# Kernel optimization log

Measured on AMD Instinct MI355X. Metric: run time of the kernel, lower is better.

The kernel has to match this reference:

```python
import jax, jax.numpy as jnp
import numpy as np

B, C, H, W = 4, 256, 48, 48
HEADS, DH = 8, 32
INNER = HEADS * DH
HID = 128  # max(16, INNER//2)
SCALE = DH ** -0.5
EPS = 1e-6


def setup_inputs() -> dict:
    key = jax.random.key(0)
    ks = jax.random.split(key, 32)
    s = 0.02
    inp = {
        'x': jax.random.normal(ks[0], (B, C, H, W), jnp.float32),
        'rgb_input': jax.random.uniform(ks[1], (B, 3, H, W), jnp.float32),
        'wq': jax.random.normal(ks[2], (INNER, C), jnp.float32) * s,
        'bq': jnp.zeros((INNER,), jnp.float32),
        'wk': jax.random.normal(ks[3], (INNER, C), jnp.float32) * s,
        'bk': jnp.zeros((INNER,), jnp.float32),
        'wv': jax.random.normal(ks[4], (INNER, C), jnp.float32) * s,
        'bv': jnp.zeros((INNER,), jnp.float32),
        'wproj': jax.random.normal(ks[5], (C, INNER), jnp.float32) * s,
        'bproj': jnp.zeros((C,), jnp.float32),
        'c1_w': jax.random.normal(ks[6], (HID, 1, 3, 3), jnp.float32) * s,
        'c1_b': jnp.zeros((HID,), jnp.float32),
        'c2_w': jax.random.normal(ks[7], (HID, HID, 3, 3), jnp.float32) * s,
        'c2_b': jnp.zeros((HID,), jnp.float32),
        'gq_w': jax.random.normal(ks[8], (INNER, HID), jnp.float32) * s,
        'gq_b': jnp.ones((INNER,), jnp.float32),
        'bqf_w': jax.random.normal(ks[9], (INNER, HID), jnp.float32) * s,
        'bqf_b': jnp.zeros((INNER,), jnp.float32),
        'gk_w': jax.random.normal(ks[10], (INNER, HID), jnp.float32) * s,
        'gk_b': jnp.ones((INNER,), jnp.float32),
        'bkf_w': jax.random.normal(ks[11], (INNER, HID), jnp.float32) * s,
        'bkf_b': jnp.zeros((INNER,), jnp.float32),
        'gv_w': jax.random.normal(ks[12], (INNER, HID), jnp.float32) * s,
        'gv_b': jnp.ones((INNER,), jnp.float32),
        'bvf_w': jax.random.normal(ks[13], (INNER, HID), jnp.float32) * s,
        'bvf_b': jnp.zeros((INNER,), jnp.float32),
        'alpha': jnp.float32(0.1),
    }
    return inp


def _conv3(x, w, b):
    y = jax.lax.conv_general_dilated(x, w, (1, 1), 'SAME',
                                     dimension_numbers=('NCHW', 'OIHW', 'NCHW'))
    return y + b[None, :, None, None]


def _rgb_to_luma(rgb):
    y = 0.299 * rgb[:, 0:1] + 0.587 * rgb[:, 1:2] + 0.114 * rgb[:, 2:3]
    y_min = jnp.min(y, axis=(2, 3), keepdims=True)
    y_max = jnp.max(y, axis=(2, 3), keepdims=True)
    return (y - y_min) / (y_max - y_min + EPS)


def reference(x, rgb_input, wq, bq, wk, bk, wv, bv, wproj, bproj,
              c1_w, c1_b, c2_w, c2_b,
              gq_w, gq_b, bqf_w, bqf_b, gk_w, gk_b, bkf_w, bkf_b,
              gv_w, gv_b, bvf_w, bvf_b, alpha):
    Bx, Cx, Hx, Wx = x.shape
    N = Hx * Wx
    luma = _rgb_to_luma(rgb_input)  # [B,1,H,W]

    # LumaCond trunk + FiLM params (1x1 convs then global spatial mean)
    h = jax.nn.relu(_conv3(luma, c1_w, c1_b))
    h = jax.nn.relu(_conv3(h, c2_w, c2_b))
    hm = h.mean(axis=(2, 3))  # [B,HID] (mean commutes with 1x1 conv)

    def film_params(gw, gb, bw, bb):
        g = hm @ gw.T + gb  # [B, INNER]
        bta = hm @ bw.T + bb
        return (g.reshape(Bx, HEADS, DH, 1), bta.reshape(Bx, HEADS, DH, 1))

    gq, fbq = film_params(gq_w, gq_b, bqf_w, bqf_b)
    gk, fbk = film_params(gk_w, gk_b, bkf_w, bkf_b)
    gv, fbv = film_params(gv_w, gv_b, bvf_w, bvf_b)

    def proj_film(w, b, g, bta):
        t = jnp.einsum('bchw,oc->bohw', x, w) + b[None, :, None, None]
        t = t.reshape(Bx, HEADS, DH, N)
        return g * t + bta  # [B,heads,dh,N]

    q = proj_film(wq, bq, gq, fbq)
    k = proj_film(wk, bk, gk, fbk)
    v = proj_film(wv, bv, gv, fbv)

    logits = jnp.einsum('bhdn,bhdm->bhnm', q, k) * SCALE  # [B,heads,N,N]

    # luma bias: avg-pooled inverse luma, mean-centered per image
    invL = 1.0 - luma
    invL = jax.lax.reduce_window(invL, 0.0, jax.lax.add,
                                 (1, 1, 3, 3), (1, 1, 1, 1), 'SAME') / 9.0
    invL = invL.reshape(Bx, N)
    invL = invL - invL.mean(axis=-1, keepdims=True)
    logits = logits + alpha * invL[:, None, None, :]

    attn = jax.nn.softmax(logits, axis=-1)
    out = jnp.einsum('bhnm,bhdm->bhdn', attn, v)  # [B,heads,dh,N]
    out = out.reshape(Bx, INNER, Hx, Wx)
    return jnp.einsum('bchw,oc->bohw', out, wproj) + bproj[None, :, None, None]
```

## Files before the change

kernel.cpp:

```cpp
#include <hip/hip_runtime.h>


#define NSP 2304
#define WID 48

typedef __attribute__((ext_vector_type(4))) float  fvec4;
typedef __attribute__((ext_vector_type(2))) unsigned int uvec2;
typedef __attribute__((ext_vector_type(4))) unsigned int uvec4;
typedef __attribute__((ext_vector_type(8))) short  short8;
typedef __attribute__((ext_vector_type(4))) float  f32x4;

__device__ inline unsigned short f2bf(float f){
  unsigned int u = __builtin_bit_cast(unsigned int, f);
  u += 0x7fffu + ((u >> 16) & 1u);
  return (unsigned short)(u >> 16);
}
__device__ inline unsigned pack2bf(float a, float b){
#if __has_builtin(__builtin_amdgcn_cvt_pk_bf16_f32)
  typedef __attribute__((ext_vector_type(2))) __bf16 bf16x2;
  bf16x2 r = __builtin_amdgcn_cvt_pk_bf16_f32(a, b);
  return __builtin_bit_cast(unsigned, r);
#else
  return (unsigned)f2bf(a) | ((unsigned)f2bf(b) << 16);
#endif
}

__global__ void k0b_wcast(const float* __restrict__ c2w, const float* __restrict__ wq,
                          const float* __restrict__ wk, const float* __restrict__ wv_,
                          const float* __restrict__ wproj,
                          unsigned short* __restrict__ wtb,
                          unsigned short* __restrict__ wqkvb,
                          unsigned short* __restrict__ wprojb){
  int idx = blockIdx.x*256 + threadIdx.x;
  if (idx < 147456){
    int ic = idx & 127, rem = idx >> 7;
    int oc = rem & 127, tap = rem >> 7;
    wtb[idx] = f2bf(c2w[(oc*128 + ic)*9 + tap]);
  } else if (idx < 344064){
    int j = idx - 147456;
    int mat = j >> 16, oc_ = j & 65535;
    const float* src = (mat == 0) ? wq : (mat == 1) ? wk : wv_;
    wqkvb[j] = f2bf(src[oc_]);
  } else {
    int j = idx - 344064;
    wprojb[j] = f2bf(wproj[j]);
  }
}

__global__ __launch_bounds__(256) void k0xt(const float* __restrict__ x,
                                            unsigned short* __restrict__ xt){
  int nt = blockIdx.x, cc = blockIdx.y, b = blockIdx.z, t = threadIdx.x;
  __shared__ unsigned short tb[64*72];
  int cl0 = t >> 4;
  int nl0 = (t & 15) * 4;
  #pragma unroll
  for (int ps = 0; ps < 4; ++ps){
    int cl = cl0 + ps*16;
    fvec4 v = *(const fvec4*)(x + ((size_t)(b*256 + cc*64 + cl))*NSP + nt*64 + nl0);
    #pragma unroll
    for (int i = 0; i < 4; ++i) tb[(nl0+i)*72 + cl] = f2bf(v[i]);
  }
  __syncthreads();
  int nl = t >> 2, cg = (t & 3) * 16;
  uvec4 u0 = *(const uvec4*)&tb[nl*72 + cg];
  uvec4 u1 = *(const uvec4*)&tb[nl*72 + cg + 8];
  unsigned short* dst = xt + ((size_t)(b*NSP + nt*64 + nl))*256 + cc*64 + cg;
  *(uvec4*)dst = u0;
  *(uvec4*)(dst + 8) = u1;
}

__global__ void k1_luma(const float* __restrict__ rgb, const float* __restrict__ alphaP,
                        float* __restrict__ luma_n, float* __restrict__ bias_a,
                        float* __restrict__ hm_sum){
  int b = blockIdx.x, t = threadIdx.x;
  __shared__ float ly[NSP];
  __shared__ float ll[NSP];
  __shared__ float red[256];
  __shared__ float red2[256];
  const float* rp = rgb + b*3*NSP;
  float lmin = 1e30f, lmax = -1e30f;
  for (int i = t; i < NSP; i += 256){
    float y = 0.299f*rp[i] + 0.587f*rp[NSP+i] + 0.114f*rp[2*NSP+i];
    ly[i] = y; lmin = fminf(lmin, y); lmax = fmaxf(lmax, y);
  }
  red[t] = lmin; red2[t] = lmax;
  __syncthreads();
  for (int s = 128; s > 0; s >>= 1){
    if (t < s){ red[t] = fminf(red[t], red[t+s]); red2[t] = fmaxf(red2[t], red2[t+s]); }
    __syncthreads();
  }
  float mn = red[0], mx = red2[0];
  float inv = 1.0f / (mx - mn + 1e-6f);
  for (int i = t; i < NSP; i += 256){
    float v = (ly[i] - mn) * inv;
    ll[i] = v;
    luma_n[b*NSP + i] = v;
  }
  if (t < 128) hm_sum[b*128 + t] = 0.f;
  __syncthreads();
  float pr[9]; float psum = 0.f;
  #pragma unroll
  for (int ii = 0; ii < 9; ++ii){
    int n = t + 256*ii;
    int row = n / WID, col = n - row*WID;
    float s = 0.f;
    #pragma unroll
    for (int dy = -1; dy <= 1; ++dy)
      #pragma unroll
      for (int dx = -1; dx <= 1; ++dx){
        int r2 = row+dy, c2 = col+dx;
        if (r2 >= 0 && r2 < WID && c2 >= 0 && c2 < WID) s += 1.0f - ll[r2*WID + c2];
      }
    pr[ii] = s * (1.f/9.f);
    psum += pr[ii];
  }
  __syncthreads();
  red[t] = psum;
  __syncthreads();
  for (int s = 128; s > 0; s >>= 1){
    if (t < s) red[t] += red[t+s];
    __syncthreads();
  }
  float mean = red[0] * (1.f/(float)NSP);
  float alpha = alphaP[0] * 1.4426950408889634f;
  #pragma unroll
  for (int ii = 0; ii < 9; ++ii){
    int n = t + 256*ii;
    bias_a[b*NSP + n] = alpha * (pr[ii] - mean);
  }
}

__global__ void k2_conv1(const float* __restrict__ luma_n, const float* __restrict__ c1w,
                         const float* __restrict__ c1b, unsigned short* __restrict__ h1p){
  int nt = blockIdx.x, ocg = blockIdx.y, b = blockIdx.z, t = threadIdx.x;
  __shared__ float wsm[32*9];
  __shared__ float bsm[32];
  for (int i = t; i < 288; i += 256) wsm[i] = c1w[ocg*288 + i];
  if (t < 32) bsm[t] = c1b[ocg*32 + t];
  __syncthreads();
  int n = nt*256 + t;
  int row = n / WID, col = n - row*WID;
  const float* lp = luma_n + b*NSP;
  float lv[9];
  int k = 0;
  #pragma unroll
  for (int dy = -1; dy <= 1; ++dy)
    #pragma unroll
    for (int dx = -1; dx <= 1; ++dx, ++k){
      int r2 = row+dy, c2 = col+dx;
      lv[k] = (r2 >= 0 && r2 < WID && c2 >= 0 && c2 < WID) ? lp[r2*WID + c2] : 0.f;
    }
  unsigned int packed[16];
  #pragma unroll
  for (int oc2 = 0; oc2 < 16; ++oc2){
    float a0 = bsm[oc2*2], a1 = bsm[oc2*2+1];
    #pragma unroll
    for (int q = 0; q < 9; ++q){
      a0 += wsm[(oc2*2)*9 + q] * lv[q];
      a1 += wsm[(oc2*2+1)*9 + q] * lv[q];
    }
    packed[oc2] = pack2bf(fmaxf(a0, 0.f), fmaxf(a1, 0.f));
  }
  unsigned short* dst = h1p + ((size_t)(b*2500 + (row+1)*50 + (col+1)))*128 + ocg*32;
  #pragma unroll
  for (int q4 = 0; q4 < 4; ++q4)
    *(uvec4*)(dst + q4*8) = *(uvec4*)&packed[q4*4];
}

__global__ __launch_bounds__(256) void k3_conv2(const unsigned short* __restrict__ h1p,
    const unsigned short* __restrict__ wtb, const float* __restrict__ c2b,
    float* __restrict__ hm_sum){
  int row = blockIdx.x, mh = blockIdx.y, b = blockIdx.z;
  int t = threadIdx.x, wv = t >> 6, lane = t & 63;
  int lq = lane >> 4, lc = lane & 15;
  int ocb = mh*64 + wv*16;
  const f32x4 z4 = {0.f, 0.f, 0.f, 0.f};
  f32x4 C[3] = {z4, z4, z4};
  const unsigned short* hbase = h1p + (size_t)b*2500*128;
  #pragma unroll
  for (int tap = 0; tap < 9; ++tap){
    int dy = tap/3 - 1, dx = tap%3 - 1;
    const unsigned short* wrow = wtb + (tap*128 + ocb + lc)*128 + lq*8;
    const unsigned short* hrow = hbase + ((row+dy+1)*50 + (dx+1) + lc)*128 + lq*8;
    #pragma unroll
    for (int kc = 0; kc < 4; ++kc){
      short8 aW = *(const short8*)(wrow + kc*32);
      #pragma unroll
      for (int ntp = 0; ntp < 3; ++ntp){
        short8 bH = *(const short8*)(hrow + ntp*16*128 + kc*32);
        C[ntp] = __builtin_amdgcn_mfma_f32_16x16x32_bf16(aW, bH, C[ntp], 0, 0, 0);
      }
    }
  }
  float s[4];
  #pragma unroll
  for (int r = 0; r < 4; ++r){
    float bias = c2b[ocb + lq*4 + r];
    float v = 0.f;
    #pragma unroll
    for (int ntp = 0; ntp < 3; ++ntp) v += fmaxf(C[ntp][r] + bias, 0.f);
    v += __shfl_xor(v, 1, 64);
    v += __shfl_xor(v, 2, 64);
    v += __shfl_xor(v, 4, 64);
    v += __shfl_xor(v, 8, 64);
    s[r] = v;
  }
  if (lc == 0){
    #pragma unroll
    for (int r = 0; r < 4; ++r)
      atomicAdd(&hm_sum[b*128 + ocb + lq*4 + r], s[r]);
  }
}

__global__ void k4_film(const float* __restrict__ hm_sum,
  const float* w0, const float* b0, const float* w1, const float* b1,
  const float* w2, const float* b2, const float* w3, const float* b3,
  const float* w4, const float* b4, const float* w5, const float* b5,
  float* __restrict__ film){
  __shared__ float hs[128];
  int bb = blockIdx.x & 3, m6 = blockIdx.x >> 2, t = threadIdx.x;
  if (t < 128) hs[t] = hm_sum[bb*128 + t] * (1.f/(float)NSP);
  __syncthreads();
  const float* wm[6] = {w0,w1,w2,w3,w4,w5};
  const float* bm[6] = {b0,b1,b2,b3,b4,b5};
  const float* w = wm[m6];
  int o = t;
  float a = bm[m6][o];
  for (int h2 = 0; h2 < 128; ++h2) a += hs[h2] * w[o*128 + h2];
  film[blockIdx.x*256 + t] = a;
}

__global__ __launch_bounds__(256) void k5_qkv(const unsigned short* __restrict__ xt,
    const unsigned short* __restrict__ wqkvb,
    const float* __restrict__ bq, const float* __restrict__ bk, const float* __restrict__ bv,
    const float* __restrict__ film,
    unsigned short* __restrict__ q_t, unsigned short* __restrict__ k_t,
    unsigned short* __restrict__ v_b){
  int nt = blockIdx.x, ot = blockIdx.y, b = blockIdx.z;
  int t = threadIdx.x, wv = t >> 6, lane = t & 63;
  int lq = lane >> 4, lc = lane & 15;
  int p = ot >> 1;
  int omb = (ot & 1)*128 + wv*32;
  const unsigned short* wb = wqkvb + p*65536;
  const f32x4 z4 = {0.f, 0.f, 0.f, 0.f};
  f32x4 acc[2][4];
  #pragma unroll
  for (int oh = 0; oh < 2; ++oh)
    #pragma unroll
    for (int nq = 0; nq < 4; ++nq) acc[oh][nq] = z4;
  for (int kc = 0; kc < 8; ++kc){
    short8 aW[2];
    #pragma unroll
    for (int oh = 0; oh < 2; ++oh)
      aW[oh] = *(const short8*)(wb + (omb + oh*16 + lc)*256 + kc*32 + lq*8);
    short8 bX[4];
    #pragma unroll
    for (int nq = 0; nq < 4; ++nq)
      bX[nq] = *(const short8*)(xt + ((size_t)(b*NSP + nt*64 + nq*16 + lc))*256 + kc*32 + lq*8);
    #pragma unroll
    for (int oh = 0; oh < 2; ++oh)
      #pragma unroll
      for (int nq = 0; nq < 4; ++nq)
        acc[oh][nq] = __builtin_amdgcn_mfma_f32_16x16x32_bf16(aW[oh], bX[nq], acc[oh][nq], 0, 0, 0);
  }
  const float* bvec = (p == 0) ? bq : (p == 1) ? bk : bv;
  int hq = omb >> 5;
  unsigned short* qk = (p == 0) ? q_t : k_t;
  #pragma unroll
  for (int oh = 0; oh < 2; ++oh){
    fvec4 g4 = *(const fvec4*)(film + (2*p*4 + b)*256 + omb + oh*16 + lq*4);
    fvec4 t4 = *(const fvec4*)(film + ((2*p+1)*4 + b)*256 + omb + oh*16 + lq*4);
    fvec4 z4b = *(const fvec4*)(bvec + omb + oh*16 + lq*4);
    #pragma unroll
    for (int nq = 0; nq < 4; ++nq){
      int n = nt*64 + nq*16 + lc;
      float v0 = g4[0]*(acc[oh][nq][0] + z4b[0]) + t4[0];
      float v1 = g4[1]*(acc[oh][nq][1] + z4b[1]) + t4[1];
      float v2 = g4[2]*(acc[oh][nq][2] + z4b[2]) + t4[2];
      float v3 = g4[3]*(acc[oh][nq][3] + z4b[3]) + t4[3];
      if (p == 0){
        const float sc = 0.17677669529663687f * 1.4426950408889634f;
        v0 *= sc; v1 *= sc; v2 *= sc; v3 *= sc;
      }
      if (p < 2){
        uvec2 u;
        u.x = pack2bf(v0, v1);
        u.y = pack2bf(v2, v3);
        *(uvec2*)(qk + ((size_t)((b*8 + hq)*NSP + n))*32 + oh*16 + lq*4) = u;
      } else {
        int om = omb + oh*16 + lq*4;
        v_b[((size_t)(b*256 + om + 0))*NSP + n] = f2bf(v0);
        v_b[((size_t)(b*256 + om + 1))*NSP + n] = f2bf(v1);
        v_b[((size_t)(b*256 + om + 2))*NSP + n] = f2bf(v2);
        v_b[((size_t)(b*256 + om + 3))*NSP + n] = f2bf(v3);
      }
    }
  }
}

__global__ __launch_bounds__(256, 4) void k6_attn(const unsigned short* __restrict__ q_t,
    const unsigned short* __restrict__ k_t, const unsigned short* __restrict__ v_b,
    const float* __restrict__ bias_a,
    unsigned short* __restrict__ o0, unsigned short* __restrict__ o1,
    float* __restrict__ l0, float* __restrict__ l1){
  int bx = blockIdx.x, h = blockIdx.y, b = blockIdx.z;
  int qblk = bx >> 1, s = bx & 1;
  unsigned short* op = s ? o1 : o0;
  float* lp = s ? l1 : l0;
  int t = threadIdx.x, wv = t >> 6, lane = t & 63;
  int lq = lane >> 4, lc = lane & 15;
  int bh = b*8 + h;
  int nb0 = qblk*128 + wv*32;
  const f32x4 z4 = {0.f, 0.f, 0.f, 0.f};
  int ms = s*1152;

  __shared__ unsigned short Kb[2][64*32];
  __shared__ unsigned short Vb[2][32*64];
  __shared__ float ps[4][1024];

  const unsigned short* kg = k_t + ((size_t)bh*NSP + ms + (t>>2))*32 + (t&3)*8;
  const unsigned short* vg = v_b + ((size_t)(b*256 + h*32 + (t>>3)))*NSP + ms + (t&7)*8;
  int krow = t >> 2;
  unsigned short* kw = &Kb[0][krow*32 + (((t&3) ^ ((krow>>1)&3))*8)];
  int vrow = t >> 3;
  unsigned short* vw = &Vb[0][vrow*64 + (((t&7) ^ (vrow&7))*8)];

  int kcol = (lq ^ ((lc>>1)&3))*8;
  int sxm = ((lc&7)<<2) | (((lc>>3)&1)<<1);
  int wbase = lc*32;

  const float* brow = bias_a + b*NSP + ms;
  fvec4 c0r[4];
  #pragma unroll
  for (int g = 0; g < 4; ++g) c0r[g] = *(const fvec4*)(brow + g*16 + lq*4);

  short8 aQ[2];
  #pragma unroll
  for (int qf = 0; qf < 2; ++qf)
    aQ[qf] = *(const short8*)(q_t + ((size_t)(bh*NSP + nb0 + qf*16 + lc))*32 + lq*8);

  uvec4 gKr = *(const uvec4*)kg;
  uvec4 gVr = *(const uvec4*)vg;

  const uvec4 onesu = {0x3F803F80u, 0x3F803F80u, 0x3F803F80u, 0x3F803F80u};
  const short8 aOnes = __builtin_bit_cast(short8, onesu);

  f32x4 O[2][2]; f32x4 Ol[2];
  #pragma unroll
  for (int qf = 0; qf < 2; ++qf){
    Ol[qf] = z4; O[qf][0] = z4; O[qf][1] = z4;
  }
  float* myps = ps[wv];

  for (int it = 0; it < 18; ++it){
    int buf = it & 1;
    *(uvec4*)(kw + buf*2048) = gKr;
    *(uvec4*)(vw + buf*2048) = gVr;
    __syncthreads();
    if (it < 17){
      gKr = *(const uvec4*)(kg + (it+1)*2048);
      gVr = *(const uvec4*)(vg + (it+1)*64);
    }
    const unsigned short* kb = Kb[buf];
    const unsigned short* vb = Vb[buf];
    short8 aK[4], aV[2][2];
    #pragma unroll
    for (int g = 0; g < 4; ++g)
      aK[g] = *(const short8*)(kb + (g*16 + lc)*32 + kcol);
    #pragma unroll
    for (int dhg = 0; dhg < 2; ++dhg)
      #pragma unroll
      for (int mh = 0; mh < 2; ++mh)
        aV[dhg][mh] = *(const short8*)(vb + (dhg*16 + lc)*64 + (((mh*4 + lq) ^ (lc&7))*8));
    #pragma unroll
    for (int qf = 0; qf < 2; ++qf){
      #pragma unroll
      for (int g = 0; g < 4; ++g){
        f32x4 S = __builtin_amdgcn_mfma_f32_16x16x32_bf16(aK[g], aQ[qf], c0r[g], 0, 0, 0);
        uvec2 w2;
        w2.x = pack2bf(__builtin_amdgcn_exp2f(S[0]), __builtin_amdgcn_exp2f(S[1]));
        w2.y = pack2bf(__builtin_amdgcn_exp2f(S[2]), __builtin_amdgcn_exp2f(S[3]));
        *(uvec2*)&myps[qf*512 + wbase + ((g*8 + lq*2) ^ sxm)] = w2;
      }
    }
    if (it < 17){
      #pragma unroll
      for (int g = 0; g < 4; ++g)
        c0r[g] = *(const fvec4*)(brow + (it+1)*64 + g*16 + lq*4);
    }
    __builtin_amdgcn_s_setprio(1);
    #pragma unroll
    for (int qf = 0; qf < 2; ++qf){
      #pragma unroll
      for (int mh = 0; mh < 2; ++mh){
        int d0 = (mh*16 + lq*4) ^ sxm;
        uvec2 lo = *(const uvec2*)&myps[qf*512 + wbase + d0];
        uvec2 hi = *(const uvec2*)&myps[qf*512 + wbase + (d0 ^ 2)];
        uvec4 up; up.x = lo.x; up.y = lo.y; up.z = hi.x; up.w = hi.y;
        short8 bP = __builtin_bit_cast(short8, up);
        Ol[qf] = __builtin_amdgcn_mfma_f32_16x16x32_bf16(aOnes, bP, Ol[qf], 0, 0, 0);
        #pragma unroll
        for (int dhg = 0; dhg < 2; ++dhg)
          O[qf][dhg] = __builtin_amdgcn_mfma_f32_16x16x32_bf16(aV[dhg][mh], bP, O[qf][dhg], 0, 0, 0);
      }
    }
    __builtin_amdgcn_s_setprio(0);
  }
  #pragma unroll
  for (int qf = 0; qf < 2; ++qf){
    int nidx = nb0 + qf*16 + lc;
    if (lq == 0) lp[b*NSP + nidx] = Ol[qf][0];
    #pragma unroll
    for (int dh = 0; dh < 2; ++dh){
      uvec2 u;
      u.x = pack2bf(O[qf][dh][0], O[qf][dh][1]);
      u.y = pack2bf(O[qf][dh][2], O[qf][dh][3]);
      *(uvec2*)(op + ((size_t)(b*NSP + nidx))*256 + h*32 + dh*16 + lq*4) = u;
    }
  }
}

__global__ __launch_bounds__(256) void k7_proj(const unsigned short* __restrict__ a0,
    const unsigned short* __restrict__ a1, const float* __restrict__ l0p,
    const float* __restrict__ l1p, const unsigned short* __restrict__ wprojb,
    const float* __restrict__ bproj, float* __restrict__ out){
  int nt = blockIdx.x, ct = blockIdx.y, b = blockIdx.z;
  int t = threadIdx.x, wv = t >> 6, lane = t & 63;
  int lq = lane >> 4, lc = lane & 15;
  __shared__ float rls[32];
  if (t < 32) rls[t] = 1.0f / (l0p[b*NSP + nt*32 + t] + l1p[b*NSP + nt*32 + t]);
  __syncthreads();
  int cb = ct*128 + wv*32;
  const f32x4 z4 = {0.f, 0.f, 0.f, 0.f};
  f32x4 acc[2][2];
  #pragma unroll
  for (int ch = 0; ch < 2; ++ch)
    #pragma unroll
    for (int nq = 0; nq < 2; ++nq) acc[ch][nq] = z4;
  for (int kc = 0; kc < 8; ++kc){
    short8 aW[2];
    #pragma unroll
    for (int ch = 0; ch < 2; ++ch)
      aW[ch] = *(const short8*)(wprojb + (cb + ch*16 + lc)*256 + kc*32 + lq*8);
    #pragma unroll
    for (int src = 0; src < 2; ++src){
      const unsigned short* ap = src ? a1 : a0;
      short8 bA[2];
      #pragma unroll
      for (int nq = 0; nq < 2; ++nq)
        bA[nq] = *(const short8*)(ap + ((size_t)(b*NSP + nt*32 + nq*16 + lc))*256 + kc*32 + lq*8);
      #pragma unroll
      for (int ch = 0; ch < 2; ++ch)
        #pragma unroll
        for (int nq = 0; nq < 2; ++nq)
          acc[ch][nq] = __builtin_amdgcn_mfma_f32_16x16x32_bf16(aW[ch], bA[nq], acc[ch][nq], 0, 0, 0);
    }
  }
  #pragma unroll
  for (int ch = 0; ch < 2; ++ch){
    #pragma unroll
    for (int nq = 0; nq < 2; ++nq){
      int n = nt*32 + nq*16 + lc;
      float rl = rls[nq*16 + lc];
      #pragma unroll
      for (int r = 0; r < 4; ++r){
        int c = cb + ch*16 + lq*4 + r;
        out[((size_t)(b*256 + c))*NSP + n] = acc[ch][nq][r]*rl + bproj[c];
      }
    }
  }
}

extern "C" void kernel_launch(void* const* d_in, const int* in_sizes, int n_in,
                              void* d_out, int out_size, void* d_ws, size_t ws_size,
                              hipStream_t stream) {
  const float* x     = (const float*)d_in[0];
  const float* rgb   = (const float*)d_in[1];
  const float* wq    = (const float*)d_in[2];
  const float* bq    = (const float*)d_in[3];
  const float* wk    = (const float*)d_in[4];
  const float* bk    = (const float*)d_in[5];
  const float* wv    = (const float*)d_in[6];
  const float* bv    = (const float*)d_in[7];
  const float* wproj = (const float*)d_in[8];
  const float* bproj = (const float*)d_in[9];
  const float* c1w   = (const float*)d_in[10];
  const float* c1b   = (const float*)d_in[11];
  const float* c2w   = (const float*)d_in[12];
  const float* c2b   = (const float*)d_in[13];
  const float* gq_w  = (const float*)d_in[14];
  const float* gq_b  = (const float*)d_in[15];
  const float* bqf_w = (const float*)d_in[16];
  const float* bqf_b = (const float*)d_in[17];
  const float* gk_w  = (const float*)d_in[18];
  const float* gk_b  = (const float*)d_in[19];
  const float* bkf_w = (const float*)d_in[20];
  const float* bkf_b = (const float*)d_in[21];
  const float* gv_w  = (const float*)d_in[22];
  const float* gv_b  = (const float*)d_in[23];
  const float* bvf_w = (const float*)d_in[24];
  const float* bvf_b = (const float*)d_in[25];
  const float* alphaP= (const float*)d_in[26];

  char* w = (char*)d_ws;
  float* luma_n = (float*)w;            w += 4*NSP*4;
  float* bias_a = (float*)w;            w += 4*NSP*4;
  float* hm_sum = (float*)w;            w += 512*4;
  float* film   = (float*)w;            w += 6*4*256*4;
  unsigned short* h1p = (unsigned short*)w; w += 4*2500*128*2;
  unsigned short* wtb = (unsigned short*)w; w += 9*128*128*2;
  unsigned short* wqkvb = (unsigned short*)w; w += 3*256*256*2;
  unsigned short* wprojb = (unsigned short*)w; w += 256*256*2;
  unsigned short* xt  = (unsigned short*)w; w += (size_t)4*NSP*256*2;
  unsigned short* q_t = (unsigned short*)w; w += (size_t)4*8*NSP*32*2;
  unsigned short* k_t = (unsigned short*)w; w += (size_t)4*8*NSP*32*2;
  unsigned short* v_b = (unsigned short*)w; w += (size_t)4*256*NSP*2;
  unsigned short* o_part0 = (unsigned short*)w; w += (size_t)4*NSP*256*2;
  unsigned short* o_part1 = (unsigned short*)w; w += (size_t)4*NSP*256*2;
  float* l_part0 = (float*)w;           w += 4*NSP*4;
  float* l_part1 = (float*)w;           w += 4*NSP*4;

  (void)hipMemsetAsync(h1p, 0, (size_t)4*2500*128*2, stream);
  k0b_wcast<<<1600, 256, 0, stream>>>(c2w, wq, wk, wv, wproj, wtb, wqkvb, wprojb);
  k0xt    <<<dim3(36,4,4), 256, 0, stream>>>(x, xt);
  k1_luma <<<4, 256, 0, stream>>>(rgb, alphaP, luma_n, bias_a, hm_sum);
  k2_conv1<<<dim3(9,4,4), 256, 0, stream>>>(luma_n, c1w, c1b, h1p);
  k3_conv2<<<dim3(48,2,4), 256, 0, stream>>>(h1p, wtb, c2b, hm_sum);
  k4_film <<<24, 256, 0, stream>>>(hm_sum, gq_w, gq_b, bqf_w, bqf_b,
                                   gk_w, gk_b, bkf_w, bkf_b,
                                   gv_w, gv_b, bvf_w, bvf_b, film);
  k5_qkv  <<<dim3(36,6,4), 256, 0, stream>>>(xt, wqkvb, bq, bk, bv, film,
                                             q_t, k_t, v_b);
  k6_attn <<<dim3(36,8,4), 256, 0, stream>>>(q_t, k_t, v_b, bias_a,
                                             o_part0, o_part1, l_part0, l_part1);
  k7_proj <<<dim3(72,2,4), 256, 0, stream>>>(o_part0, o_part1, l_part0, l_part1,
                                             wprojb, bproj, (float*)d_out);
}
```

Measured before the change: 267.5 us.

## Register-prefetch operands in GEMMs, drop LDS staging in attention, fold halo memset into luma

```diff
diff --git a/kernel.cpp b/kernel.cpp
--- a/kernel.cpp
+++ b/kernel.cpp
@@ -69,64 +69,80 @@
   *(uvec4*)(dst + 8) = u1;
 }
 
-__global__ void k1_luma(const float* __restrict__ rgb, const float* __restrict__ alphaP,
+__global__ __launch_bounds__(1024) void k1_luma(const float* __restrict__ rgb,
+                        const float* __restrict__ alphaP,
                         float* __restrict__ luma_n, float* __restrict__ bias_a,
-                        float* __restrict__ hm_sum){
+                        float* __restrict__ hm_sum, unsigned short* __restrict__ h1p){
   int b = blockIdx.x, t = threadIdx.x;
   __shared__ float ly[NSP];
   __shared__ float ll[NSP];
-  __shared__ float red[256];
-  __shared__ float red2[256];
+  __shared__ float red[1024];
+  __shared__ float red2[1024];
+  {
+    const uvec4 z = {0u,0u,0u,0u};
+    for (int j = t; j < 196*16; j += 1024){
+      int cell = j >> 4, q = j & 15;
+      int r, c;
+      if (cell < 50)      { r = 0;           c = cell; }
+      else if (cell < 100){ r = 49;          c = cell - 50; }
+      else if (cell < 148){ r = cell - 99;   c = 0; }
+      else                { r = cell - 147;  c = 49; }
+      *(uvec4*)(h1p + ((size_t)(b*2500 + r*50 + c))*128 + q*8) = z;
+    }
+  }
   const float* rp = rgb + b*3*NSP;
   float lmin = 1e30f, lmax = -1e30f;
-  for (int i = t; i < NSP; i += 256){
+  for (int i = t; i < NSP; i += 1024){
     float y = 0.299f*rp[i] + 0.587f*rp[NSP+i] + 0.114f*rp[2*NSP+i];
     ly[i] = y; lmin = fminf(lmin, y); lmax = fmaxf(lmax, y);
   }
   red[t] = lmin; red2[t] = lmax;
   __syncthreads();
-  for (int s = 128; s > 0; s >>= 1){
+  for (int s = 512; s > 0; s >>= 1){
     if (t < s){ red[t] = fminf(red[t], red[t+s]); red2[t] = fmaxf(red2[t], red2[t+s]); }
     __syncthreads();
   }
   float mn = red[0], mx = red2[0];
   float inv = 1.0f / (mx - mn + 1e-6f);
-  for (int i = t; i < NSP; i += 256){
+  for (int i = t; i < NSP; i += 1024){
     float v = (ly[i] - mn) * inv;
     ll[i] = v;
     luma_n[b*NSP + i] = v;
   }
   if (t < 128) hm_sum[b*128 + t] = 0.f;
   __syncthreads();
-  float pr[9]; float psum = 0.f;
-  #pragma unroll
-  for (int ii = 0; ii < 9; ++ii){
-    int n = t + 256*ii;
-    int row = n / WID, col = n - row*WID;
-    float s = 0.f;
-    #pragma unroll
-    for (int dy = -1; dy <= 1; ++dy)
-      #pragma unroll
-      for (int dx = -1; dx <= 1; ++dx){
-        int r2 = row+dy, c2 = col+dx;
-        if (r2 >= 0 && r2 < WID && c2 >= 0 && c2 < WID) s += 1.0f - ll[r2*WID + c2];
-      }
-    pr[ii] = s * (1.f/9.f);
-    psum += pr[ii];
+  float pr[3]; float psum = 0.f;
+  #pragma unroll
+  for (int ii = 0; ii < 3; ++ii){
+    int n = t + 1024*ii;
+    pr[ii] = 0.f;
+    if (n < NSP){
+      int row = n / WID, col = n - row*WID;
+      float s = 0.f;
+      #pragma unroll
+      for (int dy = -1; dy <= 1; ++dy)
+        #pragma unroll
+        for (int dx = -1; dx <= 1; ++dx){
+          int r2 = row+dy, c2 = col+dx;
+          if (r2 >= 0 && r2 < WID && c2 >= 0 && c2 < WID) s += 1.0f - ll[r2*WID + c2];
+        }
+      pr[ii] = s * (1.f/9.f);
+      psum += pr[ii];
+    }
   }
   __syncthreads();
   red[t] = psum;
   __syncthreads();
-  for (int s = 128; s > 0; s >>= 1){
+  for (int s = 512; s > 0; s >>= 1){
     if (t < s) red[t] += red[t+s];
     __syncthreads();
   }
   float mean = red[0] * (1.f/(float)NSP);
   float alpha = alphaP[0] * 1.4426950408889634f;
   #pragma unroll
-  for (int ii = 0; ii < 9; ++ii){
-    int n = t + 256*ii;
-    bias_a[b*NSP + n] = alpha * (pr[ii] - mean);
+  for (int ii = 0; ii < 3; ++ii){
+    int n = t + 1024*ii;
+    if (n < NSP) bias_a[b*NSP + n] = alpha * (pr[ii] - mean);
   }
 }
 
@@ -241,28 +257,41 @@
   int lq = lane >> 4, lc = lane & 15;
   int p = ot >> 1;
   int omb = (ot & 1)*128 + wv*32;
-  const unsigned short* wb = wqkvb + p*65536;
   const f32x4 z4 = {0.f, 0.f, 0.f, 0.f};
   f32x4 acc[2][4];
   #pragma unroll
   for (int oh = 0; oh < 2; ++oh)
     #pragma unroll
     for (int nq = 0; nq < 4; ++nq) acc[oh][nq] = z4;
-  for (int kc = 0; kc < 8; ++kc){
-    short8 aW[2];
+
+  const unsigned short* wbp = wqkvb + p*65536 + (omb + lc)*256 + lq*8;
+  const unsigned short* xbp = xt + ((size_t)(b*NSP + nt*64 + lc))*256 + lq*8;
+
+  short8 aW0[2], aW1[2], bX0[4], bX1[4];
+  auto loadW = [&](short8 (&W)[2], int kc){
+    #pragma unroll
+    for (int oh = 0; oh < 2; ++oh) W[oh] = *(const short8*)(wbp + oh*16*256 + kc*32);
+  };
+  auto loadX = [&](short8 (&X)[4], int kc){
+    #pragma unroll
+    for (int nq = 0; nq < 4; ++nq) X[nq] = *(const short8*)(xbp + (size_t)nq*16*256 + kc*32);
+  };
+  auto mm = [&](short8 (&W)[2], short8 (&X)[4]){
     #pragma unroll
     for (int oh = 0; oh < 2; ++oh)
-      aW[oh] = *(const short8*)(wb + (omb + oh*16 + lc)*256 + kc*32 + lq*8);
-    short8 bX[4];
-    #pragma unroll
-    for (int nq = 0; nq < 4; ++nq)
-      bX[nq] = *(const short8*)(xt + ((size_t)(b*NSP + nt*64 + nq*16 + lc))*256 + kc*32 + lq*8);
-    #pragma unroll
-    for (int oh = 0; oh < 2; ++oh)
       #pragma unroll
       for (int nq = 0; nq < 4; ++nq)
-        acc[oh][nq] = __builtin_amdgcn_mfma_f32_16x16x32_bf16(aW[oh], bX[nq], acc[oh][nq], 0, 0, 0);
-  }
+        acc[oh][nq] = __builtin_amdgcn_mfma_f32_16x16x32_bf16(W[oh], X[nq], acc[oh][nq], 0, 0, 0);
+  };
+  loadW(aW0, 0); loadX(bX0, 0);
+  for (int kc2 = 0; kc2 < 4; ++kc2){
+    loadW(aW1, kc2*2+1); loadX(bX1, kc2*2+1);
+    mm(aW0, bX0);
+    int kn = (kc2*2+2) & 7;
+    loadW(aW0, kn); loadX(bX0, kn);
+    mm(aW1, bX1);
+  }
+
   const float* bvec = (p == 0) ? bq : (p == 1) ? bk : bv;
   int hq = omb >> 5;
   unsigned short* qk = (p == 0) ? q_t : k_t;
@@ -314,33 +343,23 @@
   const f32x4 z4 = {0.f, 0.f, 0.f, 0.f};
   int ms = s*1152;
 
-  __shared__ unsigned short Kb[2][64*32];
-  __shared__ unsigned short Vb[2][32*64];
   __shared__ float ps[4][1024];
-
-  const unsigned short* kg = k_t + ((size_t)bh*NSP + ms + (t>>2))*32 + (t&3)*8;
-  const unsigned short* vg = v_b + ((size_t)(b*256 + h*32 + (t>>3)))*NSP + ms + (t&7)*8;
-  int krow = t >> 2;
-  unsigned short* kw = &Kb[0][krow*32 + (((t&3) ^ ((krow>>1)&3))*8)];
-  int vrow = t >> 3;
-  unsigned short* vw = &Vb[0][vrow*64 + (((t&7) ^ (vrow&7))*8)];
-
-  int kcol = (lq ^ ((lc>>1)&3))*8;
+  float* myps = ps[wv];
   int sxm = ((lc&7)<<2) | (((lc>>3)&1)<<1);
   int wbase = lc*32;
 
+  const unsigned short* kfr = k_t + ((size_t)(bh*NSP + ms + lc))*32 + lq*8;
+  const unsigned short* vfr = v_b + ((size_t)(b*256 + h*32 + lc))*NSP + ms + lq*8;
   const float* brow = bias_a + b*NSP + ms;
-  fvec4 c0r[4];
-  #pragma unroll
-  for (int g = 0; g < 4; ++g) c0r[g] = *(const fvec4*)(brow + g*16 + lq*4);
 
   short8 aQ[2];
   #pragma unroll
   for (int qf = 0; qf < 2; ++qf)
     aQ[qf] = *(const short8*)(q_t + ((size_t)(bh*NSP + nb0 + qf*16 + lc))*32 + lq*8);
 
-  uvec4 gKr = *(const uvec4*)kg;
-  uvec4 gVr = *(const uvec4*)vg;
+  fvec4 c0r[4];
+  #pragma unroll
+  for (int g = 0; g < 4; ++g) c0r[g] = *(const fvec4*)(brow + g*16 + lq*4);
 
   const uvec4 onesu = {0x3F803F80u, 0x3F803F80u, 0x3F803F80u, 0x3F803F80u};
   const short8 aOnes = __builtin_bit_cast(short8, onesu);
@@ -350,33 +369,25 @@
   for (int qf = 0; qf < 2; ++qf){
     Ol[qf] = z4; O[qf][0] = z4; O[qf][1] = z4;
   }
-  float* myps = ps[wv];
-
-  for (int it = 0; it < 18; ++it){
-    int buf = it & 1;
-    *(uvec4*)(kw + buf*2048) = gKr;
-    *(uvec4*)(vw + buf*2048) = gVr;
-    __syncthreads();
-    if (it < 17){
-      gKr = *(const uvec4*)(kg + (it+1)*2048);
-      gVr = *(const uvec4*)(vg + (it+1)*64);
-    }
-    const unsigned short* kb = Kb[buf];
-    const unsigned short* vb = Vb[buf];
-    short8 aK[4], aV[2][2];
-    #pragma unroll
-    for (int g = 0; g < 4; ++g)
-      aK[g] = *(const short8*)(kb + (g*16 + lc)*32 + kcol);
+
+  short8 aKA[4], aKB[4];
+  #pragma unroll
+  for (int g = 0; g < 4; ++g)
+    aKA[g] = *(const short8*)(kfr + (size_t)g*512);
+
+  auto body = [&](short8 (&AK)[4], int it){
+    int m0 = it*64;
+    short8 aV[2][2];
     #pragma unroll
     for (int dhg = 0; dhg < 2; ++dhg)
       #pragma unroll
       for (int mh = 0; mh < 2; ++mh)
-        aV[dhg][mh] = *(const short8*)(vb + (dhg*16 + lc)*64 + (((mh*4 + lq) ^ (lc&7))*8));
+        aV[dhg][mh] = *(const short8*)(vfr + (size_t)dhg*16*NSP + m0 + mh*32);
     #pragma unroll
     for (int qf = 0; qf < 2; ++qf){
       #pragma unroll
       for (int g = 0; g < 4; ++g){
-        f32x4 S = __builtin_amdgcn_mfma_f32_16x16x32_bf16(aK[g], aQ[qf], c0r[g], 0, 0, 0);
+        f32x4 S = __builtin_amdgcn_mfma_f32_16x16x32_bf16(AK[g], aQ[qf], c0r[g], 0, 0, 0);
         uvec2 w2;
         w2.x = pack2bf(__builtin_amdgcn_exp2f(S[0]), __builtin_amdgcn_exp2f(S[1]));
         w2.y = pack2bf(__builtin_amdgcn_exp2f(S[2]), __builtin_amdgcn_exp2f(S[3]));
@@ -405,7 +416,20 @@
       }
     }
     __builtin_amdgcn_s_setprio(0);
-  }
+  };
+
+  for (int it2 = 0; it2 < 9; ++it2){
+    int it0 = it2*2;
+    #pragma unroll
+    for (int g = 0; g < 4; ++g)
+      aKB[g] = *(const short8*)(kfr + (size_t)(it0+1)*2048 + (size_t)g*512);
+    body(aKA, it0);
+    #pragma unroll
+    for (int g = 0; g < 4; ++g)
+      aKA[g] = *(const short8*)(kfr + (size_t)(it0+2)*2048 + (size_t)g*512);
+    body(aKB, it0+1);
+  }
+
   #pragma unroll
   for (int qf = 0; qf < 2; ++qf){
     int nidx = nb0 + qf*16 + lc;
@@ -437,25 +461,39 @@
   for (int ch = 0; ch < 2; ++ch)
     #pragma unroll
     for (int nq = 0; nq < 2; ++nq) acc[ch][nq] = z4;
-  for (int kc = 0; kc < 8; ++kc){
-    short8 aW[2];
+
+  const unsigned short* wpp = wprojb + (cb + lc)*256 + lq*8;
+  const unsigned short* a0p = a0 + ((size_t)(b*NSP + nt*32 + lc))*256 + lq*8;
+  const unsigned short* a1p = a1 + ((size_t)(b*NSP + nt*32 + lc))*256 + lq*8;
+
+  short8 W0[2], W1[2], p00[2], p01[2], p10[2], p11[2];
+  auto loadS = [&](short8 (&W)[2], short8 (&B0)[2], short8 (&B1)[2], int kc){
+    #pragma unroll
+    for (int ch = 0; ch < 2; ++ch) W[ch] = *(const short8*)(wpp + ch*16*256 + kc*32);
+    #pragma unroll
+    for (int nq = 0; nq < 2; ++nq){
+      B0[nq] = *(const short8*)(a0p + (size_t)nq*16*256 + kc*32);
+      B1[nq] = *(const short8*)(a1p + (size_t)nq*16*256 + kc*32);
+    }
+  };
+  auto mmS = [&](short8 (&W)[2], short8 (&B0)[2], short8 (&B1)[2]){
     #pragma unroll
     for (int ch = 0; ch < 2; ++ch)
-      aW[ch] = *(const short8*)(wprojb + (cb + ch*16 + lc)*256 + kc*32 + lq*8);
-    #pragma unroll
-    for (int src = 0; src < 2; ++src){
-      const unsigned short* ap = src ? a1 : a0;
-      short8 bA[2];
-      #pragma unroll
-      for (int nq = 0; nq < 2; ++nq)
-        bA[nq] = *(const short8*)(ap + ((size_t)(b*NSP + nt*32 + nq*16 + lc))*256 + kc*32 + lq*8);
-      #pragma unroll
-      for (int ch = 0; ch < 2; ++ch)
-        #pragma unroll
-        for (int nq = 0; nq < 2; ++nq)
-          acc[ch][nq] = __builtin_amdgcn_mfma_f32_16x16x32_bf16(aW[ch], bA[nq], acc[ch][nq], 0, 0, 0);
-    }
-  }
+      #pragma unroll
+      for (int nq = 0; nq < 2; ++nq){
+        acc[ch][nq] = __builtin_amdgcn_mfma_f32_16x16x32_bf16(W[ch], B0[nq], acc[ch][nq], 0, 0, 0);
+        acc[ch][nq] = __builtin_amdgcn_mfma_f32_16x16x32_bf16(W[ch], B1[nq], acc[ch][nq], 0, 0, 0);
+      }
+  };
+  loadS(W0, p00, p10, 0);
+  for (int kc2 = 0; kc2 < 4; ++kc2){
+    loadS(W1, p01, p11, kc2*2+1);
+    mmS(W0, p00, p10);
+    int kn = (kc2*2+2) & 7;
+    loadS(W0, p00, p10, kn);
+    mmS(W1, p01, p11);
+  }
+
   #pragma unroll
   for (int ch = 0; ch < 2; ++ch){
     #pragma unroll
@@ -520,10 +558,9 @@
   float* l_part0 = (float*)w;           w += 4*NSP*4;
   float* l_part1 = (float*)w;           w += 4*NSP*4;
 
-  (void)hipMemsetAsync(h1p, 0, (size_t)4*2500*128*2, stream);
   k0b_wcast<<<1600, 256, 0, stream>>>(c2w, wq, wk, wv, wproj, wtb, wqkvb, wprojb);
   k0xt    <<<dim3(36,4,4), 256, 0, stream>>>(x, xt);
-  k1_luma <<<4, 256, 0, stream>>>(rgb, alphaP, luma_n, bias_a, hm_sum);
+  k1_luma <<<4, 1024, 0, stream>>>(rgb, alphaP, luma_n, bias_a, hm_sum, h1p);
   k2_conv1<<<dim3(9,4,4), 256, 0, stream>>>(luma_n, c1w, c1b, h1p);
   k3_conv2<<<dim3(48,2,4), 256, 0, stream>>>(h1p, wtb, c2b, hm_sum);
   k4_film <<<24, 256, 0, stream>>>(hm_sum, gq_w, gq_b, bqf_w, bqf_b,
```

Measured after the change: 304.8 us. +14.0%, slower.
